# Kernel optimization log

Hardware: AMD Instinct MI355X
Metric: run time of the kernel (lower is better)

Reference implementation:

```python
import jax, jax.numpy as jnp
import numpy as np

T1, T2 = 234, 234
N_HEAD = 16

def _cross_mask(t1, t2):
    # Faithful to the torch code: mask is FLOAT, so torch SDPA treats it as an
    # ADDITIVE bias (+1.0 on cross-image positions and on row/col 0, +0 elsewhere).
    T = t1 + t2
    m = np.zeros((T, T), dtype=np.float32)
    m[:t1, t1:] = 1.0
    m[t1:, :t1] = 1.0
    full = np.ones((T + 1, T + 1), dtype=np.float32)
    full[1:, 1:] = m
    return jnp.asarray(full)

CROSS_MASK = _cross_mask(T1, T2)  # (469, 469) additive bias

def setup_inputs() -> dict:
    key = jax.random.key(0)
    ks = jax.random.split(key, 5)
    B, T, C = 64, T1 + T2 + 1, 1024
    s = 0.02
    return {
        "x": jax.random.normal(ks[0], (B, T, C), jnp.float32),
        "W_attn": jax.random.normal(ks[1], (C, 3 * C), jnp.float32) * s,
        "b_attn": jax.random.normal(ks[2], (3 * C,), jnp.float32) * s,
        "W_proj": jax.random.normal(ks[3], (C, C), jnp.float32) * s,
        "b_proj": jax.random.normal(ks[4], (C,), jnp.float32) * s,
    }

def reference(x, W_attn, b_attn, W_proj, b_proj):
    B, T, C = x.shape
    H = N_HEAD
    hd = C // H
    qkv = x @ W_attn + b_attn                      # (B, T, 3C)
    q, k, v = jnp.split(qkv, 3, axis=-1)
    def heads(t):                                  # (B, T, C) -> (B, H, T, hd)
        return t.reshape(B, T, H, hd).transpose(0, 2, 1, 3)
    q, k, v = heads(q), heads(k), heads(v)
    scale = 1.0 / jnp.sqrt(jnp.asarray(hd, x.dtype))
    scores = jnp.einsum('bhqd,bhkd->bhqk', q, k) * scale + CROSS_MASK[None, None]
    attn = jax.nn.softmax(scores, axis=-1)
    y = jnp.einsum('bhqk,bhkd->bhqd', attn, v)     # (B, H, T, hd)
    y = y.transpose(0, 2, 1, 3).reshape(B, T, C)
    return y @ W_proj + b_proj
```

## Files before the change

### kernel.cpp

```cpp
#include <hip/hip_runtime.h>

namespace {

constexpr int kT1   = 234;
constexpr int kT    = 469;
constexpr int kB    = 64;
constexpr int kC    = 1024;
constexpr int kH    = 16;
constexpr int kHD   = 64;
constexpr int kM    = kB * kT;
constexpr int kVPad = 480;
constexpr float kC1 = 0.125f * 1.44269504089f;
constexpr float kC2 = 1.44269504089f;
constexpr float kShift = 4.0f * 1.44269504089f;
constexpr float kMC0 = -kShift;
constexpr float kMC1 = kC2 - kShift;
constexpr float kNeg = -30000.f;

typedef _Float16 f16;
typedef __fp16   fp16x2 __attribute__((ext_vector_type(2)));
typedef _Float16 f16x8 __attribute__((ext_vector_type(8)));
typedef float    f32x4 __attribute__((ext_vector_type(4)));

__device__ __forceinline__ float fast_exp2(float x) {
#if __has_builtin(__builtin_amdgcn_exp2f)
  return __builtin_amdgcn_exp2f(x);
#else
  return __builtin_exp2f(x);
#endif
}

__device__ __forceinline__ void gload16(const void* g, void* l) {
  __builtin_amdgcn_global_load_lds(
      (const __attribute__((address_space(1))) unsigned int*)g,
      (__attribute__((address_space(3))) unsigned int*)l, 16, 0, 0);
}

__global__ __launch_bounds__(256) void cast_kernel(const float* __restrict__ in,
                                                   f16* __restrict__ out, int n4) {
  int i = blockIdx.x * blockDim.x + threadIdx.x;
  int stride = gridDim.x * blockDim.x;
  for (int j = i; j < n4; j += stride) {
    float4 v = reinterpret_cast<const float4*>(in)[j];
    union { f16 h[4]; unsigned long long u; } pk;
    pk.h[0] = (f16)v.x; pk.h[1] = (f16)v.y; pk.h[2] = (f16)v.z; pk.h[3] = (f16)v.w;
    reinterpret_cast<unsigned long long*>(out)[j] = pk.u;
  }
}

__global__ __launch_bounds__(256) void transpose_cast(const float* __restrict__ W,
                                                      f16* __restrict__ Wt,
                                                      int K0, int N0) {
  __shared__ float tile[32][33];
  int kb = blockIdx.x * 32, nb = blockIdx.y * 32;
  int tx = threadIdx.x & 31, ty = threadIdx.x >> 5;
  #pragma unroll
  for (int r = ty; r < 32; r += 8) tile[r][tx] = W[(size_t)(kb + r) * N0 + nb + tx];
  __syncthreads();
  #pragma unroll
  for (int r = ty; r < 32; r += 8) Wt[(size_t)(nb + r) * K0 + kb + tx] = (f16)tile[tx][r];
}

__global__ __launch_bounds__(256) void vtrans(const f16* __restrict__ in,
                                              f16* __restrict__ out) {
  __shared__ f16 tile[64][66];
  int bid = blockIdx.x;
  int bh = bid >> 3, tt = bid & 7;
  int t0 = tt * 64;
  int tx = threadIdx.x & 63, ty = threadIdx.x >> 6;
  const f16* src = in + (size_t)bh * kT * kHD;
  #pragma unroll
  for (int rr = ty; rr < 64; rr += 4) {
    int t = t0 + rr;
    tile[rr][tx] = (t < kT) ? src[(size_t)t * kHD + tx] : (f16)0.f;
  }
  __syncthreads();
  f16* dst = out + (size_t)bh * kHD * kVPad;
  int s = tx & 31, sub = tx >> 5;
  int tloc = sub * 32 + ((s >> 3) << 2) + (s & 3) + (((s >> 2) & 1) << 4);
  int tout = t0 + tx;
  if (tout < kVPad) {
    int pbase = tout & ~31, plo = tout & 7, pc = (tout >> 3) & 3;
    #pragma unroll
    for (int dd = ty; dd < 64; dd += 4) {
      int touts = pbase | plo | ((pc ^ ((dd >> 1) & 3)) << 3);
      dst[(size_t)dd * kVPad + touts] = tile[tloc][dd];
    }
  }
}

template <int EPI>
__global__ __launch_bounds__(512, 1) void gemm256(
    const f16* __restrict__ A, const f16* __restrict__ Bt,
    const float* __restrict__ bias,
    f16* __restrict__ qh, f16* __restrict__ kh, f16* __restrict__ vh,
    float* __restrict__ outp, int nbx, int nblocks) {
  __shared__ __align__(16) f16 SH[65536];
  const int K = 1024;
  int flat = blockIdx.x;
  int swz = (flat & 7) * (nblocks >> 3) + (flat >> 3);
  int mt = swz / nbx;
  int m0 = mt * 256, n0 = (swz - mt * nbx) * 256;
  int tid = threadIdx.x;
  int wid = tid >> 6, lane = tid & 63;
  int wm = wid >> 2, wn = wid & 3;
  int lhi = lane >> 4, llo = lane & 15;

  int ci0 = tid, ci1 = tid + 512;
  int r0 = ci0 >> 2, c0 = (ci0 & 3) ^ ((r0 >> 1) & 3);
  int r1 = ci1 >> 2, c1 = (ci1 & 3) ^ ((r1 >> 1) & 3);
  int gmA0 = m0 + r0; if (gmA0 >= kM) gmA0 = kM - 1;
  int gmA1 = m0 + r1; if (gmA1 >= kM) gmA1 = kM - 1;
  const f16* aS0 = A + (size_t)gmA0 * K + c0 * 8;
  const f16* aS1 = A + (size_t)gmA1 * K + c1 * 8;
  const f16* bS0 = Bt + (size_t)(n0 + r0) * K + c0 * 8;
  const f16* bS1 = Bt + (size_t)(n0 + r1) * K + c1 * 8;
  const int ld0 = ci0 * 8, ld1 = ci1 * 8;

  auto stage = [&](int reg, int kofs) {
    gload16(aS0 + kofs, &SH[reg + ld0]);
    gload16(aS1 + kofs, &SH[reg + ld1]);
    gload16(bS0 + kofs, &SH[32768 + reg + ld0]);
    gload16(bS1 + kofs, &SH[32768 + reg + ld1]);
  };

  int aOff[8], bOff[4];
  #pragma unroll
  for (int mi = 0; mi < 8; mi++) {
    int row = wm * 128 + mi * 16 + llo;
    aOff[mi] = row * 32 + ((lhi ^ ((row >> 1) & 3)) << 3);
  }
  #pragma unroll
  for (int ni = 0; ni < 4; ni++) {
    int row = wn * 64 + ni * 16 + llo;
    bOff[ni] = row * 32 + ((lhi ^ ((row >> 1) & 3)) << 3);
  }

  const f32x4 zero4 = {0.f, 0.f, 0.f, 0.f};
  f32x4 acc[8][4];
  #pragma unroll
  for (int mi = 0; mi < 8; mi++)
    #pragma unroll
    for (int ni = 0; ni < 4; ni++) acc[mi][ni] = zero4;

  stage(0 * 8192, 0);
  stage(1 * 8192, 32);
  stage(2 * 8192, 64);
  stage(3 * 8192, 96);

  for (int t = 0; t < 16; ++t) {
    int buf = t & 1;
    if (t < 15) asm volatile("s_waitcnt vmcnt(8)" ::: "memory");
    else        asm volatile("s_waitcnt vmcnt(4)" ::: "memory");
    __builtin_amdgcn_s_barrier();
    __builtin_amdgcn_sched_barrier(0);
    {
      int rb = (buf * 2 + 0) * 8192;
      f16x8 af[8], bf[4];
      #pragma unroll
      for (int mi = 0; mi < 8; mi++)
        af[mi] = *reinterpret_cast<const f16x8*>(&SH[rb + aOff[mi]]);
      #pragma unroll
      for (int ni = 0; ni < 4; ni++)
        bf[ni] = *reinterpret_cast<const f16x8*>(&SH[32768 + rb + bOff[ni]]);
      if (t >= 1 && t <= 14)
        stage(((buf ^ 1) * 2 + 1) * 8192, (t + 1) * 64 + 32);
      asm volatile("s_waitcnt lgkmcnt(0)" ::: "memory");
      __builtin_amdgcn_sched_barrier(0);
      __builtin_amdgcn_s_setprio(1);
      #pragma unroll
      for (int mi = 0; mi < 8; mi++)
        #pragma unroll
        for (int ni = 0; ni < 4; ni++)
          acc[mi][ni] = __builtin_amdgcn_mfma_f32_16x16x32_f16(af[mi], bf[ni], acc[mi][ni], 0, 0, 0);
      __builtin_amdgcn_s_setprio(0);
    }
    if (t < 15) asm volatile("s_waitcnt vmcnt(8)" ::: "memory");
    else        asm volatile("s_waitcnt vmcnt(0)" ::: "memory");
    __builtin_amdgcn_s_barrier();
    __builtin_amdgcn_sched_barrier(0);
    {
      int rb = (buf * 2 + 1) * 8192;
      f16x8 af[8], bf[4];
      #pragma unroll
      for (int mi = 0; mi < 8; mi++)
        af[mi] = *reinterpret_cast<const f16x8*>(&SH[rb + aOff[mi]]);
      #pragma unroll
      for (int ni = 0; ni < 4; ni++)
        bf[ni] = *reinterpret_cast<const f16x8*>(&SH[32768 + rb + bOff[ni]]);
      if (t <= 13)
        stage((buf * 2 + 0) * 8192, (t + 2) * 64);
      asm volatile("s_waitcnt lgkmcnt(0)" ::: "memory");
      __builtin_amdgcn_sched_barrier(0);
      __builtin_amdgcn_s_setprio(1);
      #pragma unroll
      for (int mi = 0; mi < 8; mi++)
        #pragma unroll
        for (int ni = 0; ni < 4; ni++)
          acc[mi][ni] = __builtin_amdgcn_mfma_f32_16x16x32_f16(af[mi], bf[ni], acc[mi][ni], 0, 0, 0);
      __builtin_amdgcn_s_setprio(0);
    }
  }

  float bsv[4];
  #pragma unroll
  for (int ni = 0; ni < 4; ni++) bsv[ni] = bias[n0 + wn * 64 + ni * 16 + llo];

  if constexpr (EPI == 0) {
    const int which = n0 >> 10;
    f16* dst = (which == 0) ? qh : (which == 1) ? kh : vh;
    const float osc = (which == 0) ? kC1 : 1.0f;
    #pragma unroll
    for (int mi = 0; mi < 8; mi++) {
      #pragma unroll
      for (int rr = 0; rr < 4; rr++) {
        int row = m0 + wm * 128 + mi * 16 + lhi * 4 + rr;
        if (row < kM) {
          int bb = row / kT;
          int t  = row - bb * kT;
          #pragma unroll
          for (int ni = 0; ni < 4; ni++) {
            int n = n0 + wn * 64 + ni * 16 + llo;
            int h = (n >> 6) & 15, d = n & 63;
            if (which == 1) d = (d & 7) | ((((d >> 3) ^ (t & 7)) & 7) << 3);
            dst[(((size_t)bb * kH + h) * kT + t) * kHD + d] =
                (f16)((acc[mi][ni][rr] + bsv[ni]) * osc);
          }
        }
      }
    }
  } else {
    #pragma unroll
    for (int mi = 0; mi < 8; mi++) {
      #pragma unroll
      for (int rr = 0; rr < 4; rr++) {
        int row = m0 + wm * 128 + mi * 16 + lhi * 4 + rr;
        if (row < kM) {
          #pragma unroll
          for (int ni = 0; ni < 4; ni++) {
            int n = n0 + wn * 64 + ni * 16 + llo;
            outp[(size_t)row * kC + n] = acc[mi][ni][rr] + bsv[ni];
          }
        }
      }
    }
  }
}

__global__ __launch_bounds__(512) void attn_kernel(
    const f16* __restrict__ qh, const f16* __restrict__ kh,
    const f16* __restrict__ vt, f16* __restrict__ y) {
  __shared__ __align__(16) f16 SH[16384];
  int tid = threadIdx.x;
  int w = tid >> 6, lane = tid & 63;
  int lhi = lane >> 4, llo = lane & 15;
  int bh = (blockIdx.x & 7) * 128 + (blockIdx.x >> 3);
  int bb = bh >> 4, h = bh & 15;
  const f16* qb = qh + (size_t)bh * kT * kHD;
  const f16* kb = kh + (size_t)bh * kT * kHD;
  const f16* vb = vt + (size_t)bh * kHD * kVPad;
  int qbase = w * 64;

  f16x8 qf[4][2];
  float mA[4], mB[4];
  #pragma unroll
  for (int rf = 0; rf < 4; rf++) {
    int qr = qbase + rf * 16 + llo;
    if (qr > kT - 1) qr = kT - 1;
    #pragma unroll
    for (int ks = 0; ks < 2; ks++)
      qf[rf][ks] = *reinterpret_cast<const f16x8*>(&qb[(size_t)qr * kHD + ks * 32 + lhi * 8]);
    int q = qbase + rf * 16 + llo;
    mA[rf] = (q == 0 || q > kT1) ? kMC1 : kMC0;
    mB[rf] = (q <= kT1) ? kMC1 : kMC0;
  }

  const bool isK = (tid < 256);
  const int vtid = tid & 255;
  const f16* kSrc = kb + (size_t)vtid * 8;
  const f16* vSrc = vb + (size_t)(vtid >> 2) * kVPad + (vtid & 3) * 8;
  const int ldsK = vtid * 8;
  const int ldsV = 2048 + vtid * 8;

  int kOff[2][2], vOff[4];
  #pragma unroll
  for (int kf = 0; kf < 2; kf++)
    #pragma unroll
    for (int ks = 0; ks < 2; ks++)
      kOff[kf][ks] = (kf * 16 + llo) * 64 + (((ks * 4 + lhi) ^ (llo & 7)) << 3);
  #pragma unroll
  for (int d = 0; d < 4; d++)
    vOff[d] = 2048 + (d * 16 + llo) * 32 + ((lhi ^ ((llo >> 1) & 3)) << 3);

  const f32x4 zero4 = {0.f, 0.f, 0.f, 0.f};
  f32x4 O[4][4];
  float lp[4] = {0.f, 0.f, 0.f, 0.f};
  #pragma unroll
  for (int rf = 0; rf < 4; rf++)
    #pragma unroll
    for (int d = 0; d < 4; d++) O[rf][d] = zero4;

  auto stage = [&](int t) {
    int reg = (t & 3) * 4096;
    if (isK) gload16(kSrc + (size_t)t * 2048, &SH[reg + ldsK]);
    else     gload16(vSrc + t * 32,           &SH[reg + ldsV]);
  };

  stage(0);
  stage(1);
  stage(2);

  for (int t = 0; t < 15; ++t) {
    if (t < 13)       asm volatile("s_waitcnt vmcnt(2)" ::: "memory");
    else if (t == 13) asm volatile("s_waitcnt vmcnt(1)" ::: "memory");
    else              asm volatile("s_waitcnt vmcnt(0)" ::: "memory");
    __builtin_amdgcn_s_barrier();
    __builtin_amdgcn_sched_barrier(0);
    if (t <= 11) stage(t + 3);
    int reg = (t & 3) * 4096;
    f16x8 kfr[2][2], vfr[4];
    #pragma unroll
    for (int kf = 0; kf < 2; kf++)
      #pragma unroll
      for (int ks = 0; ks < 2; ks++)
        kfr[kf][ks] = *reinterpret_cast<const f16x8*>(&SH[reg + kOff[kf][ks]]);
    __builtin_amdgcn_sched_barrier(0);
    #pragma unroll
    for (int d = 0; d < 4; d++)
      vfr[d] = *reinterpret_cast<const f16x8*>(&SH[reg + vOff[d]]);
    __builtin_amdgcn_sched_barrier(0);
    asm volatile("s_waitcnt lgkmcnt(4)" ::: "memory");
    __builtin_amdgcn_sched_barrier(0);

    f32x4 s[2][4];
    #pragma unroll
    for (int rf = 0; rf < 4; rf++) {
      float a = mA[rf], b = mB[rf];
      f32x4 sa = {a, a, a, a}, sb = {b, b, b, b};
      f32x4 s0, s1;
      if (t == 0) {
        s0 = sa; if (lhi == 0) s0[0] = kMC1;
        s1 = sa;
      } else if (t < 7) { s0 = sa; s1 = sa; }
      else if (t == 7) {
        f32x4 mix = {a, a, a, b};
        s0 = (lhi <= 1) ? sa : (lhi == 2) ? mix : sb;
        s1 = sb;
      } else if (t < 14) { s0 = sb; s1 = sb; }
      else {
        s0 = sb;
        f32x4 mix = {b, kNeg, kNeg, kNeg};
        f32x4 nng = {kNeg, kNeg, kNeg, kNeg};
        s1 = (lhi == 0) ? sb : (lhi == 1) ? mix : nng;
      }
      s[0][rf] = s0; s[1][rf] = s1;
    }

    __builtin_amdgcn_s_setprio(1);
    #pragma unroll
    for (int ks = 0; ks < 2; ks++)
      #pragma unroll
      for (int kf = 0; kf < 2; kf++)
        #pragma unroll
        for (int rf = 0; rf < 4; rf++)
          s[kf][rf] = __builtin_amdgcn_mfma_f32_16x16x32_f16(
              kfr[kf][ks], qf[rf][ks], s[kf][rf], 0, 0, 0);
    __builtin_amdgcn_s_setprio(0);

    f16x8 pa[4];
    #pragma unroll
    for (int rf = 0; rf < 4; rf++) {
      float p0 = fast_exp2(s[0][rf][0]), p1 = fast_exp2(s[0][rf][1]);
      float p2 = fast_exp2(s[0][rf][2]), p3 = fast_exp2(s[0][rf][3]);
      float p4 = fast_exp2(s[1][rf][0]), p5 = fast_exp2(s[1][rf][1]);
      float p6 = fast_exp2(s[1][rf][2]), p7 = fast_exp2(s[1][rf][3]);
      lp[rf] += ((p0 + p1) + (p2 + p3)) + ((p4 + p5) + (p6 + p7));
      union { fp16x2 h2[4]; f16x8 v; } u;
      u.h2[0] = __builtin_amdgcn_cvt_pkrtz(p0, p1);
      u.h2[1] = __builtin_amdgcn_cvt_pkrtz(p2, p3);
      u.h2[2] = __builtin_amdgcn_cvt_pkrtz(p4, p5);
      u.h2[3] = __builtin_amdgcn_cvt_pkrtz(p6, p7);
      pa[rf] = u.v;
    }

    asm volatile("s_waitcnt lgkmcnt(0)" ::: "memory");
    __builtin_amdgcn_sched_barrier(0);
    __builtin_amdgcn_s_setprio(1);
    #pragma unroll
    for (int d = 0; d < 4; d++)
      #pragma unroll
      for (int rf = 0; rf < 4; rf++)
        O[rf][d] = __builtin_amdgcn_mfma_f32_16x16x32_f16(pa[rf], vfr[d], O[rf][d], 0, 0, 0);
    __builtin_amdgcn_s_setprio(0);
  }

  #pragma unroll
  for (int rf = 0; rf < 4; rf++) {
    float l = lp[rf];
    l += __shfl_xor(l, 16, 64);
    l += __shfl_xor(l, 32, 64);
    #pragma unroll
    for (int r = 0; r < 4; r++) {
      float lr = __shfl(l, lhi * 4 + r, 64);
      int qi = qbase + rf * 16 + lhi * 4 + r;
      if (qi < kT) {
        float inv = 1.0f / lr;
        size_t base = ((size_t)bb * kT + qi) * kC + h * kHD;
        #pragma unroll
        for (int d = 0; d < 4; d++)
          y[base + d * 16 + llo] = (f16)(O[rf][d][r] * inv);
      }
    }
  }
}

}

extern "C" void kernel_launch(void* const* d_in, const int* in_sizes, int n_in,
                              void* d_out, int out_size, void* d_ws, size_t ws_size,
                              hipStream_t stream) {
  const float* x  = (const float*)d_in[0];
  const float* Wa = (const float*)d_in[1];
  const float* ba = (const float*)d_in[2];
  const float* Wp = (const float*)d_in[3];
  const float* bp = (const float*)d_in[4];
  float* out = (float*)d_out;
  char* ws = (char*)d_ws;

  const size_t sz_xh = (size_t)kM * kC * 2;
  const size_t sz_wa = (size_t)3072 * 1024 * 2;
  const size_t sz_wp = (size_t)1024 * 1024 * 2;
  const size_t sz_q  = (size_t)kB * kH * kT * kHD * 2;

  f16* xh  = (f16*)(ws);
  f16* WaT = (f16*)(ws + sz_xh);
  f16* WpT = (f16*)(ws + sz_xh + sz_wa);
  f16* qh  = (f16*)(ws + sz_xh + sz_wa + sz_wp);
  f16* kh2 = (f16*)(ws + sz_xh + sz_wa + sz_wp + sz_q);
  f16* vtt = (f16*)(ws + sz_xh + sz_wa + sz_wp + 2 * sz_q);
  f16* yh  = xh;
  f16* vtmp = (f16*)d_out;

  cast_kernel<<<2048, 256, 0, stream>>>(x, xh, kM * kC / 4);
  transpose_cast<<<dim3(32, 96), 256, 0, stream>>>(Wa, WaT, 1024, 3072);
  transpose_cast<<<dim3(32, 32), 256, 0, stream>>>(Wp, WpT, 1024, 1024);
  gemm256<0><<<118 * 12, 512, 0, stream>>>(xh, WaT, ba, qh, kh2, vtmp, nullptr, 12, 118 * 12);
  vtrans<<<kB * kH * 8, 256, 0, stream>>>(vtmp, vtt);
  attn_kernel<<<kB * kH, 512, 0, stream>>>(qh, kh2, vtt, yh);
  gemm256<1><<<118 * 4, 512, 0, stream>>>(yh, WpT, bp, nullptr, nullptr, nullptr, out, 4, 118 * 4);
}
```

Before: 520.3 us.

## Split GEMM main loop into ping-pong half-tile phases with barrier interleaving

Restructures the GEMM K-loop so each 32-wide K sub-tile is processed in two halves of the M fragments. LDS fragment loads for one half are interleaved with MFMA on the other, with extra workgroup barriers separating the phases. The prefetch depth drops from four staged sub-tiles to three, and the vmcnt waits are moved to match. The aim is finer-grained overlap of LDS reads, global staging and MFMA work across waves, in the style of a ping-pong schedule. The cost is more barriers per iteration and less global-load lookahead.

```diff
diff --git a/kernel.cpp b/kernel.cpp
--- a/kernel.cpp
+++ b/kernel.cpp
@@ -146,60 +146,84 @@
   stage(0 * 8192, 0);
   stage(1 * 8192, 32);
   stage(2 * 8192, 64);
-  stage(3 * 8192, 96);
+  asm volatile("s_waitcnt vmcnt(4)" ::: "memory");
+  __builtin_amdgcn_s_barrier();
 
   for (int t = 0; t < 16; ++t) {
     int buf = t & 1;
-    if (t < 15) asm volatile("s_waitcnt vmcnt(8)" ::: "memory");
-    else        asm volatile("s_waitcnt vmcnt(4)" ::: "memory");
-    __builtin_amdgcn_s_barrier();
-    __builtin_amdgcn_sched_barrier(0);
-    {
-      int rb = (buf * 2 + 0) * 8192;
-      f16x8 af[8], bf[4];
-      #pragma unroll
-      for (int mi = 0; mi < 8; mi++)
-        af[mi] = *reinterpret_cast<const f16x8*>(&SH[rb + aOff[mi]]);
+    const int rb0 = (buf * 2 + 0) * 8192;
+    const int rb1 = (buf * 2 + 1) * 8192;
+    f16x8 af[4], af2[4], bf[4];
+    #pragma unroll
+    for (int mi = 0; mi < 4; mi++)
+      af[mi] = *reinterpret_cast<const f16x8*>(&SH[rb0 + aOff[mi]]);
+    #pragma unroll
+    for (int ni = 0; ni < 4; ni++)
+      bf[ni] = *reinterpret_cast<const f16x8*>(&SH[32768 + rb0 + bOff[ni]]);
+    if (t <= 14) stage(((buf ^ 1) * 2 + 1) * 8192, (t + 1) * 64 + 32);
+    __builtin_amdgcn_sched_barrier(0);
+    __builtin_amdgcn_s_barrier();
+    asm volatile("s_waitcnt lgkmcnt(0)" ::: "memory");
+    __builtin_amdgcn_sched_barrier(0);
+    __builtin_amdgcn_s_setprio(1);
+    #pragma unroll
+    for (int mi = 0; mi < 4; mi++)
       #pragma unroll
       for (int ni = 0; ni < 4; ni++)
-        bf[ni] = *reinterpret_cast<const f16x8*>(&SH[32768 + rb + bOff[ni]]);
-      if (t >= 1 && t <= 14)
-        stage(((buf ^ 1) * 2 + 1) * 8192, (t + 1) * 64 + 32);
-      asm volatile("s_waitcnt lgkmcnt(0)" ::: "memory");
-      __builtin_amdgcn_sched_barrier(0);
-      __builtin_amdgcn_s_setprio(1);
-      #pragma unroll
-      for (int mi = 0; mi < 8; mi++)
-        #pragma unroll
-        for (int ni = 0; ni < 4; ni++)
-          acc[mi][ni] = __builtin_amdgcn_mfma_f32_16x16x32_f16(af[mi], bf[ni], acc[mi][ni], 0, 0, 0);
-      __builtin_amdgcn_s_setprio(0);
-    }
-    if (t < 15) asm volatile("s_waitcnt vmcnt(8)" ::: "memory");
-    else        asm volatile("s_waitcnt vmcnt(0)" ::: "memory");
-    __builtin_amdgcn_s_barrier();
-    __builtin_amdgcn_sched_barrier(0);
-    {
-      int rb = (buf * 2 + 1) * 8192;
-      f16x8 af[8], bf[4];
-      #pragma unroll
-      for (int mi = 0; mi < 8; mi++)
-        af[mi] = *reinterpret_cast<const f16x8*>(&SH[rb + aOff[mi]]);
+        acc[mi][ni] = __builtin_amdgcn_mfma_f32_16x16x32_f16(af[mi], bf[ni], acc[mi][ni], 0, 0, 0);
+    __builtin_amdgcn_s_setprio(0);
+    __builtin_amdgcn_s_barrier();
+    #pragma unroll
+    for (int mi = 0; mi < 4; mi++)
+      af2[mi] = *reinterpret_cast<const f16x8*>(&SH[rb0 + aOff[mi + 4]]);
+    __builtin_amdgcn_sched_barrier(0);
+    __builtin_amdgcn_s_barrier();
+    asm volatile("s_waitcnt lgkmcnt(0)" ::: "memory");
+    __builtin_amdgcn_sched_barrier(0);
+    __builtin_amdgcn_s_setprio(1);
+    #pragma unroll
+    for (int mi = 0; mi < 4; mi++)
       #pragma unroll
       for (int ni = 0; ni < 4; ni++)
-        bf[ni] = *reinterpret_cast<const f16x8*>(&SH[32768 + rb + bOff[ni]]);
-      if (t <= 13)
-        stage((buf * 2 + 0) * 8192, (t + 2) * 64);
-      asm volatile("s_waitcnt lgkmcnt(0)" ::: "memory");
-      __builtin_amdgcn_sched_barrier(0);
-      __builtin_amdgcn_s_setprio(1);
-      #pragma unroll
-      for (int mi = 0; mi < 8; mi++)
-        #pragma unroll
-        for (int ni = 0; ni < 4; ni++)
-          acc[mi][ni] = __builtin_amdgcn_mfma_f32_16x16x32_f16(af[mi], bf[ni], acc[mi][ni], 0, 0, 0);
-      __builtin_amdgcn_s_setprio(0);
-    }
+        acc[mi + 4][ni] = __builtin_amdgcn_mfma_f32_16x16x32_f16(af2[mi], bf[ni], acc[mi + 4][ni], 0, 0, 0);
+    __builtin_amdgcn_s_setprio(0);
+    __builtin_amdgcn_s_barrier();
+    #pragma unroll
+    for (int mi = 0; mi < 4; mi++)
+      af[mi] = *reinterpret_cast<const f16x8*>(&SH[rb1 + aOff[mi]]);
+    #pragma unroll
+    for (int ni = 0; ni < 4; ni++)
+      bf[ni] = *reinterpret_cast<const f16x8*>(&SH[32768 + rb1 + bOff[ni]]);
+    if (t <= 13) stage(rb0, (t + 2) * 64);
+    __builtin_amdgcn_sched_barrier(0);
+    __builtin_amdgcn_s_barrier();
+    asm volatile("s_waitcnt lgkmcnt(0)" ::: "memory");
+    __builtin_amdgcn_sched_barrier(0);
+    __builtin_amdgcn_s_setprio(1);
+    #pragma unroll
+    for (int mi = 0; mi < 4; mi++)
+      #pragma unroll
+      for (int ni = 0; ni < 4; ni++)
+        acc[mi][ni] = __builtin_amdgcn_mfma_f32_16x16x32_f16(af[mi], bf[ni], acc[mi][ni], 0, 0, 0);
+    __builtin_amdgcn_s_setprio(0);
+    __builtin_amdgcn_s_barrier();
+    #pragma unroll
+    for (int mi = 0; mi < 4; mi++)
+      af2[mi] = *reinterpret_cast<const f16x8*>(&SH[rb1 + aOff[mi + 4]]);
+    if (t <= 13)      asm volatile("s_waitcnt vmcnt(4)" ::: "memory");
+    else if (t == 14) asm volatile("s_waitcnt vmcnt(0)" ::: "memory");
+    __builtin_amdgcn_sched_barrier(0);
+    __builtin_amdgcn_s_barrier();
+    asm volatile("s_waitcnt lgkmcnt(0)" ::: "memory");
+    __builtin_amdgcn_sched_barrier(0);
+    __builtin_amdgcn_s_setprio(1);
+    #pragma unroll
+    for (int mi = 0; mi < 4; mi++)
+      #pragma unroll
+      for (int ni = 0; ni < 4; ni++)
+        acc[mi + 4][ni] = __builtin_amdgcn_mfma_f32_16x16x32_f16(af2[mi], bf[ni], acc[mi + 4][ni], 0, 0, 0);
+    __builtin_amdgcn_s_setprio(0);
+    __builtin_amdgcn_s_barrier();
   }
 
   float bsv[4];
```

Result: no change. 526.6 us (+1.2%).

## Fuse prep casts into one launch and deepen attention K/V pipeline to six stages

Applied to the files above, without the earlier changes.

The x cast and both weight transpose-casts are merged into one prep kernel launch, with blocks picking their job by block index, which removes two kernel launches and lets the three jobs run side by side. In the attention kernel the LDS ring grows from 4 to 6 slots. Each barrier now covers two tiles, staged and processed in pairs, which halves the number of block-wide barriers and keeps more loads in flight. This uses more LDS per block (48KB) and so may reduce occupancy.

```diff
diff --git a/kernel.cpp b/kernel.cpp
--- a/kernel.cpp
+++ b/kernel.cpp
@@ -36,29 +36,33 @@
       (__attribute__((address_space(3))) unsigned int*)l, 16, 0, 0);
 }
 
-__global__ __launch_bounds__(256) void cast_kernel(const float* __restrict__ in,
-                                                   f16* __restrict__ out, int n4) {
-  int i = blockIdx.x * blockDim.x + threadIdx.x;
-  int stride = gridDim.x * blockDim.x;
-  for (int j = i; j < n4; j += stride) {
-    float4 v = reinterpret_cast<const float4*>(in)[j];
-    union { f16 h[4]; unsigned long long u; } pk;
-    pk.h[0] = (f16)v.x; pk.h[1] = (f16)v.y; pk.h[2] = (f16)v.z; pk.h[3] = (f16)v.w;
-    reinterpret_cast<unsigned long long*>(out)[j] = pk.u;
-  }
-}
-
-__global__ __launch_bounds__(256) void transpose_cast(const float* __restrict__ W,
-                                                      f16* __restrict__ Wt,
-                                                      int K0, int N0) {
+__global__ __launch_bounds__(256) void prep_kernel(
+    const float* __restrict__ x, f16* __restrict__ xh,
+    const float* __restrict__ Wa, f16* __restrict__ WaT,
+    const float* __restrict__ Wp, f16* __restrict__ WpT, int n4) {
   __shared__ float tile[32][33];
-  int kb = blockIdx.x * 32, nb = blockIdx.y * 32;
+  int b = blockIdx.x;
+  if (b < 2048) {
+    int i = b * blockDim.x + threadIdx.x;
+    int stride = 2048 * blockDim.x;
+    for (int j = i; j < n4; j += stride) {
+      float4 v = reinterpret_cast<const float4*>(x)[j];
+      union { f16 h[4]; unsigned long long u; } pk;
+      pk.h[0] = (f16)v.x; pk.h[1] = (f16)v.y; pk.h[2] = (f16)v.z; pk.h[3] = (f16)v.w;
+      reinterpret_cast<unsigned long long*>(xh)[j] = pk.u;
+    }
+    return;
+  }
+  const float* W; f16* Wt; int N0, i;
+  if (b < 5120) { W = Wa; Wt = WaT; N0 = 3072; i = b - 2048; }
+  else          { W = Wp; Wt = WpT; N0 = 1024; i = b - 5120; }
+  int kb = (i & 31) * 32, nb = (i >> 5) * 32;
   int tx = threadIdx.x & 31, ty = threadIdx.x >> 5;
   #pragma unroll
   for (int r = ty; r < 32; r += 8) tile[r][tx] = W[(size_t)(kb + r) * N0 + nb + tx];
   __syncthreads();
   #pragma unroll
-  for (int r = ty; r < 32; r += 8) Wt[(size_t)(nb + r) * K0 + kb + tx] = (f16)tile[tx][r];
+  for (int r = ty; r < 32; r += 8) Wt[(size_t)(nb + r) * 1024 + kb + tx] = (f16)tile[tx][r];
 }
 
 __global__ __launch_bounds__(256) void vtrans(const f16* __restrict__ in,
@@ -250,7 +254,7 @@
 __global__ __launch_bounds__(512) void attn_kernel(
     const f16* __restrict__ qh, const f16* __restrict__ kh,
     const f16* __restrict__ vt, f16* __restrict__ y) {
-  __shared__ __align__(16) f16 SH[16384];
+  __shared__ __align__(16) f16 SH[24576];
   int tid = threadIdx.x;
   int w = tid >> 6, lane = tid & 63;
   int lhi = lane >> 4, llo = lane & 15;
@@ -301,23 +305,13 @@
     for (int d = 0; d < 4; d++) O[rf][d] = zero4;
 
   auto stage = [&](int t) {
-    int reg = (t & 3) * 4096;
+    int reg = (t % 6) * 4096;
     if (isK) gload16(kSrc + (size_t)t * 2048, &SH[reg + ldsK]);
     else     gload16(vSrc + t * 32,           &SH[reg + ldsV]);
   };
 
-  stage(0);
-  stage(1);
-  stage(2);
-
-  for (int t = 0; t < 15; ++t) {
-    if (t < 13)       asm volatile("s_waitcnt vmcnt(2)" ::: "memory");
-    else if (t == 13) asm volatile("s_waitcnt vmcnt(1)" ::: "memory");
-    else              asm volatile("s_waitcnt vmcnt(0)" ::: "memory");
-    __builtin_amdgcn_s_barrier();
-    __builtin_amdgcn_sched_barrier(0);
-    if (t <= 11) stage(t + 3);
-    int reg = (t & 3) * 4096;
+  auto process = [&](int t) {
+    int reg = (t % 6) * 4096;
     f16x8 kfr[2][2], vfr[4];
     #pragma unroll
     for (int kf = 0; kf < 2; kf++)
@@ -392,7 +386,24 @@
       for (int rf = 0; rf < 4; rf++)
         O[rf][d] = __builtin_amdgcn_mfma_f32_16x16x32_f16(pa[rf], vfr[d], O[rf][d], 0, 0, 0);
     __builtin_amdgcn_s_setprio(0);
-  }
+  };
+
+  stage(0); stage(1); stage(2); stage(3);
+
+  for (int w2 = 0; w2 < 7; ++w2) {
+    if (w2 < 6) asm volatile("s_waitcnt vmcnt(2)" ::: "memory");
+    else        asm volatile("s_waitcnt vmcnt(1)" ::: "memory");
+    __builtin_amdgcn_s_barrier();
+    __builtin_amdgcn_sched_barrier(0);
+    if (w2 <= 4)      { stage(2 * w2 + 4); stage(2 * w2 + 5); }
+    else if (w2 == 5) { stage(14); }
+    process(2 * w2);
+    process(2 * w2 + 1);
+  }
+  asm volatile("s_waitcnt vmcnt(0)" ::: "memory");
+  __builtin_amdgcn_s_barrier();
+  __builtin_amdgcn_sched_barrier(0);
+  process(14);
 
   #pragma unroll
   for (int rf = 0; rf < 4; rf++) {
@@ -441,9 +452,7 @@
   f16* yh  = xh;
   f16* vtmp = (f16*)d_out;
 
-  cast_kernel<<<2048, 256, 0, stream>>>(x, xh, kM * kC / 4);
-  transpose_cast<<<dim3(32, 96), 256, 0, stream>>>(Wa, WaT, 1024, 3072);
-  transpose_cast<<<dim3(32, 32), 256, 0, stream>>>(Wp, WpT, 1024, 1024);
+  prep_kernel<<<6144, 256, 0, stream>>>(x, xh, Wa, WaT, Wp, WpT, kM * kC / 4);
   gemm256<0><<<118 * 12, 512, 0, stream>>>(xh, WaT, ba, qh, kh2, vtmp, nullptr, 12, 118 * 12);
   vtrans<<<kB * kH * 8, 256, 0, stream>>>(vtmp, vtt);
   attn_kernel<<<kB * kH, 512, 0, stream>>>(qh, kh2, vtt, yh);
```

Result: no change. 529.2 us (+1.7%).
